# Kernel optimization log

Measured on AMD Instinct MI355X. Metric: run time of the kernel, lower is better.

The kernel has to match this reference:

```python
import jax, jax.numpy as jnp
import numpy as np

VAR0, VAR1 = 0.1, 0.2   # cfg['variance']
THRESH = 0.5            # overlap_thresh
THETA = 0.01
NEGPOS = 3


def decode(loc, priors):
    # priors center-form [P,4]; returns point-form boxes [P,4]
    cxcy = priors[:, :2] + loc[:, :2] * VAR0 * priors[:, 2:]
    wh = priors[:, 2:] * jnp.exp(loc[:, 2:] * VAR1)
    return jnp.concatenate([cxcy - wh * 0.5, cxcy + wh * 0.5], axis=1)


def center_size(b):
    return jnp.concatenate([(b[:, :2] + b[:, 2:]) * 0.5, b[:, 2:] - b[:, :2]], axis=1)


def encode(matched, priors_c):
    # matched point-form [P,4], priors_c center-form [P,4]
    g_cxcy = ((matched[:, :2] + matched[:, 2:]) * 0.5 - priors_c[:, :2]) / (VAR0 * priors_c[:, 2:])
    g_wh = jnp.log((matched[:, 2:] - matched[:, :2]) / priors_c[:, 2:]) / VAR1
    return jnp.concatenate([g_cxcy, g_wh], axis=1)


def jaccard(a, b):
    # a [G,4], b [P,4] point form -> IoU [G,P]
    lt = jnp.maximum(a[:, None, :2], b[None, :, :2])
    rb = jnp.minimum(a[:, None, 2:], b[None, :, 2:])
    wh = jnp.clip(rb - lt, 0.0)
    inter = wh[..., 0] * wh[..., 1]
    area_a = ((a[:, 2] - a[:, 0]) * (a[:, 3] - a[:, 1]))[:, None]
    area_b = ((b[:, 2] - b[:, 0]) * (b[:, 3] - b[:, 1]))[None, :]
    return inter / (area_a + area_b - inter)


def _match_one(truths, labels, gt_mask, arm_loc, priors):
    # refine_match with arm_loc (use_ARM=True path)
    P = priors.shape[0]
    G = truths.shape[0]
    dec = decode(arm_loc, priors)                                 # [P,4]
    ov = jnp.where(gt_mask[:, None], jaccard(truths, dec), -1.0)  # [G,P], padded GT masked out
    best_prior_idx = jnp.argmax(ov, axis=1)                       # [G]
    best_truth_ov = jnp.max(ov, axis=0)                           # [P]
    best_truth_idx = jnp.argmax(ov, axis=0)                       # [P]
    safe = jnp.where(gt_mask, best_prior_idx, P)                  # OOB index -> dropped scatter
    best_truth_ov = best_truth_ov.at[safe].set(2.0, mode='drop')  # force-match each valid GT
    best_truth_idx = best_truth_idx.at[safe].set(jnp.arange(G), mode='drop')
    matched = truths[best_truth_idx]                              # [P,4]
    conf = jnp.where(best_truth_ov < THRESH, 0, labels[best_truth_idx])
    loc = encode(matched, center_size(dec))
    return loc, conf


def forward(arm_loc, arm_conf, odm_loc, odm_conf, priors, targets, num_gts):
    B, P, C = odm_conf.shape
    truths = targets[..., :4]
    labels = targets[..., 4].astype(jnp.int32)
    gt_mask = jnp.arange(targets.shape[1])[None, :] < num_gts[:, None]
    loc_t, conf_t = jax.vmap(_match_one, in_axes=(0, 0, 0, 0, None))(
        truths, labels, gt_mask,
        jax.lax.stop_gradient(arm_loc), jax.lax.stop_gradient(priors))
    loc_t = jax.lax.stop_gradient(loc_t)    # loc_t.requires_grad = False
    conf_t = jax.lax.stop_gradient(conf_t)

    # ARM objectness filter on positives
    p_obj = jax.nn.softmax(arm_conf, axis=2)[:, :, 1]
    pos = (conf_t > 0) & (p_obj > THETA)

    # masked smooth-L1 localization loss (sum)
    posf = pos[..., None].astype(odm_loc.dtype)
    d = jnp.abs(odm_loc * posf - loc_t * posf)
    loss_l = jnp.sum(jnp.where(d < 1.0, 0.5 * d * d, d - 0.5))

    # hard negative mining on per-prior softmax loss
    batch_conf = odm_conf.reshape(-1, C)
    lc = jax.nn.logsumexp(batch_conf, axis=1) - jnp.take_along_axis(
        batch_conf, conf_t.reshape(-1, 1), axis=1)[:, 0]
    lc = jnp.where(pos.reshape(-1), 0.0, lc).reshape(B, P)
    loss_idx = jnp.argsort(-lc, axis=1)
    idx_rank = jnp.argsort(loss_idx, axis=1)
    num_pos = jnp.sum(pos.astype(jnp.int32), axis=1, keepdims=True)  # [B,1]
    num_neg = jnp.minimum(NEGPOS * num_pos, P - 1)
    neg = idx_rank < num_neg
    mask = pos | neg

    # masked cross entropy (compute on zeroed-out logits like the original, then mask)
    conf_p = (odm_conf * mask[..., None].astype(odm_conf.dtype)).reshape(-1, C)
    tgt = jnp.where(mask, conf_t, 0).reshape(-1)
    logp = jax.nn.log_softmax(conf_p, axis=1)
    ce = -jnp.take_along_axis(logp, tgt[:, None], axis=1)[:, 0]
    loss_c = jnp.sum(ce * mask.reshape(-1).astype(ce.dtype))

    N = jnp.sum(num_pos).astype(jnp.float32)
    return loss_l / N, loss_c / N


def setup_inputs():
    key = jax.random.key(0)
    ks = jax.random.split(key, 10)
    B, P, C, G = 32, 16320, 21, 40
    arm_loc = jax.random.normal(ks[0], (B, P, 4), jnp.float32) * 0.1
    arm_conf = jax.random.normal(ks[1], (B, P, 2), jnp.float32)
    odm_loc = jax.random.normal(ks[2], (B, P, 4), jnp.float32) * 0.1
    odm_conf = jax.random.normal(ks[3], (B, P, C), jnp.float32)
    # priors in center form with positive sizes
    pc = jax.random.uniform(ks[4], (P, 2), jnp.float32, 0.1, 0.9)
    pwh = jax.random.uniform(ks[5], (P, 2), jnp.float32, 0.05, 0.3)
    priors = jnp.concatenate([pc, pwh], axis=1)
    # GT boxes in point form with positive area, labels in 1..C-1, padded to G=40
    gc = jax.random.uniform(ks[6], (B, G, 2), jnp.float32, 0.2, 0.8)
    gwh = jax.random.uniform(ks[7], (B, G, 2), jnp.float32, 0.05, 0.3)
    boxes = jnp.concatenate([gc - gwh * 0.5, gc + gwh * 0.5], axis=-1)
    labels = jax.random.randint(ks[8], (B, G, 1), 1, C).astype(jnp.float32)
    targets = jnp.concatenate([boxes, labels], axis=-1)
    num_gts = jax.random.randint(ks[9], (B,), 1, G + 1).astype(jnp.int32)
    return {"arm_loc": arm_loc, "arm_conf": arm_conf, "odm_loc": odm_loc,
            "odm_conf": odm_conf, "priors": priors, "targets": targets,
            "num_gts": num_gts}


def reference(arm_loc, arm_conf, odm_loc, odm_conf, priors, targets, num_gts):
    return forward(arm_loc, arm_conf, odm_loc, odm_conf, priors, targets, num_gts)
```

## Files before the change

kernel.cpp:

```cpp
#include <hip/hip_runtime.h>
#include <math.h>

#define VAR0 0.1f
#define VAR1 0.2f
#define THRESH 0.5f
#define THETA 0.01f
#define MAXG 64
#define BLK 256
#define SELT 1024
#define NCH 16
#define NB 4096
#define CAP 2048

__device__ __forceinline__ float fdiv_fast(float a, float b) { return __fdividef(a, b); }

__device__ __forceinline__ float4 decode_box(float4 l, float4 pr) {
    float cx = pr.x + l.x * VAR0 * pr.z;
    float cy = pr.y + l.y * VAR0 * pr.w;
    float w = pr.z * __expf(l.z * VAR1);
    float h = pr.w * __expf(l.w * VAR1);
    return make_float4(cx - w * 0.5f, cy - h * 0.5f, cx + w * 0.5f, cy + h * 0.5f);
}

__device__ __forceinline__ float smooth_l1_sum(float4 ol, float4 t, float4 d) {
    float pcx = (d.x + d.z) * 0.5f, pcy = (d.y + d.w) * 0.5f;
    float pw = d.z - d.x, ph = d.w - d.y;
    float g0 = fdiv_fast((t.x + t.z) * 0.5f - pcx, VAR0 * pw);
    float g1 = fdiv_fast((t.y + t.w) * 0.5f - pcy, VAR0 * ph);
    float g2 = __logf(fdiv_fast(t.z - t.x, pw)) * (1.0f / VAR1);
    float g3 = __logf(fdiv_fast(t.w - t.y, ph)) * (1.0f / VAR1);
    float s = 0.f, dd;
    dd = fabsf(ol.x - g0); s += (dd < 1.f) ? 0.5f*dd*dd : dd - 0.5f;
    dd = fabsf(ol.y - g1); s += (dd < 1.f) ? 0.5f*dd*dd : dd - 0.5f;
    dd = fabsf(ol.z - g2); s += (dd < 1.f) ? 0.5f*dd*dd : dd - 0.5f;
    dd = fabsf(ol.w - g3); s += (dd < 1.f) ? 0.5f*dd*dd : dd - 0.5f;
    return s;
}

__device__ __forceinline__ float softmax_pobj(float2 c) {
    float mm = fmaxf(c.x, c.y);
    float e0 = __expf(c.x - mm), e1 = __expf(c.y - mm);
    return fdiv_fast(e1, e0 + e1);
}

__device__ __forceinline__ float iou_ov(float4 t, float areaA, float4 d, float areaB) {
    float lt0 = fmaxf(t.x, d.x), lt1 = fmaxf(t.y, d.y);
    float rb0 = fminf(t.z, d.z), rb1 = fminf(t.w, d.w);
    float w = rb0 - lt0; if (w < 0.f) w = 0.f;
    float h = rb1 - lt1; if (h < 0.f) h = 0.f;
    float inter = w * h;
    return fdiv_fast(inter, areaA + areaB - inter);
}

__device__ __forceinline__ unsigned wave_umax_bits(unsigned v) {
    int x = (int)v;
    int t;
    t = __builtin_amdgcn_update_dpp(0, x, 0x111, 0xf, 0xf, true);  x = (t > x) ? t : x;
    t = __builtin_amdgcn_update_dpp(0, x, 0x112, 0xf, 0xf, true);  x = (t > x) ? t : x;
    t = __builtin_amdgcn_update_dpp(0, x, 0x114, 0xf, 0xf, true);  x = (t > x) ? t : x;
    t = __builtin_amdgcn_update_dpp(0, x, 0x118, 0xf, 0xf, true);  x = (t > x) ? t : x;
    t = __builtin_amdgcn_update_dpp(0, x, 0x142, 0xa, 0xf, false); x = (t > x) ? t : x;
    t = __builtin_amdgcn_update_dpp(0, x, 0x143, 0xc, 0xf, false); x = (t > x) ? t : x;
    return (unsigned)__builtin_amdgcn_readlane(x, 63);
}

__global__ __launch_bounds__(BLK) void k_match(
        const float* __restrict__ arm_loc, const float* __restrict__ priors,
        const float* __restrict__ arm_conf, const float* __restrict__ odm_loc,
        const float* __restrict__ targets, const int* __restrict__ num_gts,
        unsigned char* __restrict__ posm, unsigned* __restrict__ bb,
        unsigned long long* __restrict__ bpw,
        float* __restrict__ partL, int* __restrict__ partN,
        int B, int P, int G) {
    int b = blockIdx.y;
    int p0 = blockIdx.x * BLK;
    int tid = threadIdx.x;
    int p = p0 + tid;
    int lane = tid & 63, wid = tid >> 6;
    int wavebase = p0 + (tid & ~63);
    __shared__ float4 st4[MAXG];
    __shared__ float  stl[MAXG];
    __shared__ float  sarea[MAXG];
    __shared__ unsigned long long wk[4][MAXG];
    __shared__ int sng;
    if (tid == 0) sng = num_gts[b];
    for (int g = tid; g < G; g += BLK) {
        const float* tg = targets + (size_t)b * G * 5 + g * 5;
        float t0 = tg[0], t1 = tg[1], t2 = tg[2], t3 = tg[3];
        st4[g] = make_float4(t0, t1, t2, t3);
        stl[g] = tg[4];
        sarea[g] = (t2 - t0) * (t3 - t1);
    }
    __syncthreads();
    int ng = sng;
    bool ok = p < P;
    float4 d = make_float4(0.f, 0.f, 0.f, 0.f);
    float areaB = 0.f;
    size_t i = (size_t)b * P + (ok ? p : 0);
    if (ok) {
        float4 l = ((const float4*)arm_loc)[i];
        float4 pr = ((const float4*)priors)[p];
        d = decode_box(l, pr);
        areaB = (d.z - d.x) * (d.w - d.y);
    }
    float bov = -2.0f; int bidx = 0;
    int g = 0;
    for (; g + 2 <= ng; g += 2) {
        float4 t0g = st4[g], t1g = st4[g + 1];
        unsigned vb0 = 0u, vb1 = 0u;
        if (ok) {
            float ov0 = iou_ov(t0g, sarea[g], d, areaB);
            float ov1 = iou_ov(t1g, sarea[g + 1], d, areaB);
            if (ov0 > bov) { bov = ov0; bidx = g; }
            if (ov1 > bov) { bov = ov1; bidx = g + 1; }
            vb0 = __float_as_uint(ov0);
            vb1 = __float_as_uint(ov1);
        }
        unsigned om0 = wave_umax_bits(vb0);
        unsigned om1 = wave_umax_bits(vb1);
        unsigned long long m0 = __ballot(ok && vb0 == om0);
        unsigned long long m1 = __ballot(ok && vb1 == om1);
        if (lane == 0) {
            unsigned long long k0 = 0ull, k1 = 0ull;
            if (m0) {
                int pw = wavebase + (int)__builtin_ctzll(m0);
                k0 = ((unsigned long long)om0 << 32)
                   | (unsigned long long)(0xFFFFFFFFu - (unsigned)pw);
            }
            if (m1) {
                int pw = wavebase + (int)__builtin_ctzll(m1);
                k1 = ((unsigned long long)om1 << 32)
                   | (unsigned long long)(0xFFFFFFFFu - (unsigned)pw);
            }
            wk[wid][g] = k0;
            wk[wid][g + 1] = k1;
        }
    }
    if (g < ng) {
        float4 tg = st4[g];
        unsigned vb = 0u;
        if (ok) {
            float ov = iou_ov(tg, sarea[g], d, areaB);
            if (ov > bov) { bov = ov; bidx = g; }
            vb = __float_as_uint(ov);
        }
        unsigned om = wave_umax_bits(vb);
        unsigned long long m = __ballot(ok && vb == om);
        if (lane == 0) {
            unsigned long long k0 = 0ull;
            if (m) {
                int pw = wavebase + (int)__builtin_ctzll(m);
                k0 = ((unsigned long long)om << 32)
                   | (unsigned long long)(0xFFFFFFFFu - (unsigned)pw);
            }
            wk[wid][g] = k0;
        }
    }
    float lsum = 0.f; int pc = 0;
    if (ok) {
        int conf_t = (bov < THRESH) ? 0 : (int)stl[bidx];
        float p_obj = softmax_pobj(((const float2*)arm_conf)[i]);
        bool pos = (conf_t > 0) && (p_obj > THETA);
        if (pos) {
            pc = 1;
            float4 ol = ((const float4*)odm_loc)[i];
            lsum = smooth_l1_sum(ol, st4[bidx], d);
        }
        posm[i] = pos ? 1 : 0;
        bb[i] = (__float_as_uint(bov) & 0xFFFFFFC0u) | (unsigned)bidx;
    }
    __shared__ float rl[BLK];
    __shared__ int rc[BLK];
    rl[tid] = lsum; rc[tid] = pc;
    __syncthreads();
    if (tid < ng) {
        unsigned long long k0 = wk[0][tid], k1 = wk[1][tid];
        unsigned long long k2 = wk[2][tid], k3 = wk[3][tid];
        unsigned long long m01 = k0 > k1 ? k0 : k1;
        unsigned long long m23 = k2 > k3 ? k2 : k3;
        unsigned long long m = m01 > m23 ? m01 : m23;
        bpw[(size_t)(b * G + tid) * gridDim.x + blockIdx.x] = m;
    }
    for (int off = BLK/2; off > 0; off >>= 1) {
        if (tid < off) { rl[tid] += rl[tid+off]; rc[tid] += rc[tid+off]; }
        __syncthreads();
    }
    if (tid == 0) {
        partL[b * gridDim.x + blockIdx.x] = rl[0];
        partN[b * gridDim.x + blockIdx.x] = rc[0];
    }
}

__global__ __launch_bounds__(BLK) void k_lse(
        const float* __restrict__ odm_conf, const float* __restrict__ targets,
        const unsigned* __restrict__ bb,
        float* __restrict__ ce, int B, int P, int C, int G) {
    int b = blockIdx.y;
    int p0 = blockIdx.x * BLK;
    int tid = threadIdx.x;
    int p = p0 + tid;
    __shared__ float stl[MAXG];
    __shared__ float oc_s[BLK * 21];
    for (int gg = tid; gg < G; gg += BLK) stl[gg] = targets[(size_t)b * G * 5 + gg * 5 + 4];
    int nrows = P - p0; if (nrows > BLK) nrows = BLK;
    int nf = nrows * C;
    const float* ocb = odm_conf + ((size_t)b * P + p0) * C;
    int nf4 = nf >> 2;
    const float4* ocb4 = (const float4*)ocb;
    for (int i2 = tid; i2 < nf4; i2 += BLK) ((float4*)oc_s)[i2] = ocb4[i2];
    if (tid < (nf & 3)) oc_s[(nf4 << 2) + tid] = ocb[(nf4 << 2) + tid];
    __syncthreads();
    if (p < P) {
        size_t i = (size_t)b * P + p;
        unsigned bbv = bb[i];
        int bidx = (int)(bbv & 63u);
        int conf_t = (__uint_as_float(bbv & 0xFFFFFFC0u) >= THRESH) ? (int)stl[bidx] : 0;
        const float* oc = oc_s + tid * C;
        float mx = oc[0];
        for (int j = 1; j < C; ++j) mx = fmaxf(mx, oc[j]);
        float sume = 0.f;
        for (int j = 0; j < C; ++j) sume += __expf(oc[j] - mx);
        float lse = mx + __logf(sume);
        ce[i] = lse - oc[conf_t];
    }
}

__global__ __launch_bounds__(1024) void k_fixpatch(
        const float* __restrict__ arm_loc, const float* __restrict__ priors,
        const float* __restrict__ arm_conf, const float* __restrict__ odm_loc,
        const float* __restrict__ odm_conf,
        const float* __restrict__ targets, const int* __restrict__ num_gts,
        const unsigned long long* __restrict__ bpw, const unsigned* __restrict__ bb,
        float* __restrict__ ce, unsigned char* __restrict__ posm,
        float* __restrict__ partPL, int* __restrict__ partPN,
        int B, int P, int C, int G, int NBX) {
    int b = blockIdx.x;
    int tid = threadIdx.x;
    int lane = tid & 63, wid = tid >> 6;
    __shared__ int fp[MAXG];
    __shared__ float4 st4[MAXG];
    __shared__ float  stl[MAXG];
    __shared__ int sng;
    if (tid == 0) sng = num_gts[b];
    for (int g = tid; g < G; g += 1024) {
        const float* tg = targets + (size_t)b * G * 5 + g * 5;
        st4[g] = make_float4(tg[0], tg[1], tg[2], tg[3]);
        stl[g] = tg[4];
    }
    __syncthreads();
    int ng = sng;
    for (int g = wid; g < ng; g += 16) {
        const unsigned long long* src = bpw + (size_t)(b * G + g) * NBX;
        unsigned long long key = 0ull;
        for (int j = lane; j < NBX; j += 64) {
            unsigned long long v = src[j];
            if (v > key) key = v;
        }
        for (int off = 32; off > 0; off >>= 1) {
            unsigned long long o = __shfl_down(key, (unsigned)off, 64);
            if (o > key) key = o;
        }
        if (lane == 0) fp[g] = (int)(0xFFFFFFFFu - (unsigned)(key & 0xFFFFFFFFull));
    }
    __syncthreads();
    if (tid < G) {
        float dL = 0.f; int dN = 0;
        if (tid < ng) {
            int g = tid;
            bool dup = false;
            for (int g2 = g + 1; g2 < ng; ++g2) if (fp[g2] == fp[g]) { dup = true; break; }
            if (!dup) {
                int p = fp[g];
                size_t i = (size_t)b * P + p;
                unsigned bbv = bb[i];
                int old_bidx = (int)(bbv & 63u);
                bool old_ge = __uint_as_float(bbv & 0xFFFFFFC0u) >= THRESH;
                int old_ct = old_ge ? (int)stl[old_bidx] : 0;
                int new_ct = (int)stl[g];
                float p_obj = softmax_pobj(((const float2*)arm_conf)[i]);
                bool old_pos = (old_ct > 0) && (p_obj > THETA);
                bool new_pos = (p_obj > THETA);
                if (old_pos || new_pos) {
                    float4 l = ((const float4*)arm_loc)[i];
                    float4 pr = ((const float4*)priors)[p];
                    float4 d = decode_box(l, pr);
                    float4 ol = ((const float4*)odm_loc)[i];
                    if (old_pos) dL -= smooth_l1_sum(ol, st4[old_bidx], d);
                    if (new_pos) dL += smooth_l1_sum(ol, st4[g], d);
                }
                dN = (new_pos ? 1 : 0) - (old_pos ? 1 : 0);
                const float* oc = odm_conf + i * (size_t)C;
                float ce_old = ce[i];
                float ce_new = (old_ct == new_ct) ? ce_old
                             : (ce_old + oc[old_ct] - oc[new_ct]);
                ce[i] = ce_new;
                posm[i] = new_pos ? 1 : 0;
            }
        }
        partPL[b * G + tid] = dL;
        partPN[b * G + tid] = dN;
    }
}

__global__ __launch_bounds__(SELT) void k_select(
        const float* __restrict__ ce, const unsigned char* __restrict__ posm,
        const int* __restrict__ partN, const int* __restrict__ partPN,
        const float* __restrict__ partL, const float* __restrict__ partPL,
        int NBX, int G,
        float* __restrict__ partC, float* __restrict__ totL,
        int* __restrict__ npos, int P) {
    int b = blockIdx.x;
    int tid = threadIdx.x;
    int lane = tid & 63, wid = tid >> 6;
    __shared__ unsigned hist[NB];
    __shared__ float cv[CAP];
    __shared__ int   ci[CAP];
    __shared__ int   sums[SELT];
    __shared__ int   redi[16];
    __shared__ float redf[16];
    __shared__ int sh_base[16];
    __shared__ int sh_m, sh_b1, sh_k1, sh_npos, sh_istar, sh_kk, sh_cum;
    __shared__ unsigned sh_T, sh_pref;
    __shared__ float sh_mx, sh_totl;

    int c0 = 0; float l0 = 0.f;
    for (int j = tid; j < NBX; j += SELT) { c0 += partN[b * NBX + j]; l0 += partL[b * NBX + j]; }
    for (int g = tid; g < G; g += SELT)   { c0 += partPN[b * G + g];  l0 += partPL[b * G + g]; }
    for (int off = 32; off > 0; off >>= 1) {
        c0 += __shfl_down(c0, (unsigned)off, 64);
        l0 += __shfl_down(l0, (unsigned)off, 64);
    }
    if (lane == 0) { redi[wid] = c0; redf[wid] = l0; }
    __syncthreads();
    if (tid < 64) {
        int v = (tid < 16) ? redi[tid] : 0;
        float f = (tid < 16) ? redf[tid] : 0.f;
        for (int off = 32; off > 0; off >>= 1) {
            v += __shfl_down(v, (unsigned)off, 64);
            f += __shfl_down(f, (unsigned)off, 64);
        }
        if (tid == 0) { sh_npos = v; sh_totl = f; }
    }
    __syncthreads();
    int npos_b = sh_npos;
    long K = 3L * npos_b;
    if (K > P - 1) K = P - 1;

    unsigned cb[NCH];
    unsigned lv[NCH];
    unsigned pmw = 0u;
    const unsigned* ceb = (const unsigned*)ce + (size_t)b * P;
    const unsigned char* pb = posm + (size_t)b * P;
    #pragma unroll
    for (int c = 0; c < NCH; ++c) {
        int i = c * SELT + tid;
        unsigned cbits = (i < P) ? ceb[i] : 0u;
        bool ps = (i < P) && (pb[i] != 0);
        cb[c] = cbits;
        if (ps) pmw |= (1u << c);
        lv[c] = ps ? 0u : cbits;
    }

    unsigned uT = 0xFFFFFFFFu; int istar = -1;
    if (K > 0) {
        float mx = 0.f;
        #pragma unroll
        for (int c = 0; c < NCH; ++c) mx = fmaxf(mx, __uint_as_float(lv[c]));
        for (int off = 32; off > 0; off >>= 1) mx = fmaxf(mx, __shfl_xor(mx, off, 64));
        if (lane == 0) redf[wid] = mx;
        __syncthreads();
        if (tid == 0) {
            float v = redf[0];
            for (int w = 1; w < 16; ++w) v = fmaxf(v, redf[w]);
            sh_mx = v;
        }
        __syncthreads();
        float vmax = sh_mx;
        float scale = (vmax > 0.f) ? ((float)NB / vmax) : 0.f;

        for (int j = tid; j < NB; j += SELT) hist[j] = 0u;
        __syncthreads();
        #pragma unroll
        for (int c = 0; c < NCH; ++c) {
            int i = c * SELT + tid;
            if (i < P) {
                int bn = (int)(__uint_as_float(lv[c]) * scale);
                if (bn > NB - 1) bn = NB - 1;
                atomicAdd(&hist[bn], 1u);
            }
        }
        __syncthreads();

        int s4 = (int)(hist[4*tid] + hist[4*tid+1] + hist[4*tid+2] + hist[4*tid+3]);
        sums[SELT - 1 - tid] = s4;
        __syncthreads();
        int x = sums[tid];
        int xs = x;
        for (int off = 1; off < 64; off <<= 1) {
            int o = __shfl_up(xs, (unsigned)off, 64);
            if (lane >= off) xs += o;
        }
        if (lane == 63) redi[wid] = xs;
        __syncthreads();
        if (tid < 64) {
            int v = (tid < 16) ? redi[tid] : 0;
            int vs = v;
            for (int off = 1; off < 16; off <<= 1) {
                int o = __shfl_up(vs, (unsigned)off, 64);
                if (lane >= off) vs += o;
            }
            if (tid < 16) redi[tid] = vs - v;
        }
        __syncthreads();
        int excl_rev = xs + redi[wid] - x;
        sums[tid] = excl_rev;
        __syncthreads();
        int suf = sums[SELT - 1 - tid];
        {
            int run = suf;
            for (int j = 3; j >= 0; --j) {
                int bin = 4 * tid + j;
                int h = (int)hist[bin];
                if ((long)run < K && K <= (long)run + h) { sh_b1 = bin; sh_k1 = (int)(K - run); }
                run += h;
            }
        }
        __syncthreads();
        int B1 = sh_b1, k1 = sh_k1;

        if (tid == 0) sh_m = 0;
        __syncthreads();
        #pragma unroll
        for (int c = 0; c < NCH; ++c) {
            int i = c * SELT + tid;
            if (i < P) {
                float f = __uint_as_float(lv[c]);
                int bn = (int)(f * scale);
                if (bn > NB - 1) bn = NB - 1;
                if (bn == B1) {
                    int pos = atomicAdd(&sh_m, 1);
                    if (pos < CAP) { cv[pos] = f; ci[pos] = i; }
                }
            }
        }
        __syncthreads();
        int m = sh_m;
        if (m <= CAP) {
            for (int j = tid; j < m; j += SELT) {
                float vj = cv[j]; int ij = ci[j]; int r = 0;
                for (int jj = 0; jj < m; ++jj) {
                    float vx = cv[jj];
                    r += (vx > vj || (vx == vj && ci[jj] < ij)) ? 1 : 0;
                }
                if (r == k1 - 1) { sh_T = __float_as_uint(vj); sh_istar = ij; }
            }
            __syncthreads();
            uT = sh_T; istar = sh_istar;
        } else {
            if (tid == 0) { sh_pref = 0u; sh_kk = (int)K; }
            __syncthreads();
            for (int bit = 30; bit >= 0; --bit) {
                unsigned pref = sh_pref;
                int kk = sh_kk;
                unsigned hi = pref >> (bit + 1);
                int cnt = 0;
                #pragma unroll
                for (int c = 0; c < NCH; ++c) {
                    int i = c * SELT + tid;
                    unsigned v = lv[c];
                    cnt += ((i < P) && ((v >> (bit + 1)) == hi) && ((v >> bit) & 1u)) ? 1 : 0;
                }
                for (int off = 32; off > 0; off >>= 1) cnt += __shfl_down(cnt, (unsigned)off, 64);
                if (lane == 0) redi[wid] = cnt;
                __syncthreads();
                if (tid < 64) {
                    int v = (tid < 16) ? redi[tid] : 0;
                    for (int off = 32; off > 0; off >>= 1) v += __shfl_down(v, (unsigned)off, 64);
                    if (tid == 0) {
                        if (kk <= v) sh_pref = pref | (1u << bit);
                        else sh_kk = kk - v;
                    }
                }
                __syncthreads();
            }
            unsigned T = sh_pref; int krem = sh_kk;
            if (tid == 0) { sh_istar = -1; sh_cum = 0; }
            __syncthreads();
            for (int c = 0; c < NCH; ++c) {
                int i = c * SELT + tid;
                bool eq = (i < P) && (lv[c] == T);
                unsigned long long mk = __ballot(eq);
                if (lane == 0) redi[wid] = (int)__popcll(mk);
                __syncthreads();
                if (tid < 64) {
                    int v = (tid < 16) ? redi[tid] : 0;
                    for (int off = 1; off < 16; off <<= 1) {
                        int o = __shfl_up(v, (unsigned)off, 64);
                        if (lane >= off) v += o;
                    }
                    if (tid < 16) sh_base[tid] = v;
                }
                __syncthreads();
                int cum = sh_cum;
                int base = (wid == 0) ? 0 : sh_base[wid - 1];
                if (eq) {
                    int r = cum + base + (int)__popcll(mk & ((1ull << lane) - 1ull));
                    if (r == krem - 1) sh_istar = i;
                }
                __syncthreads();
                if (tid == 0) sh_cum = cum + sh_base[15];
                __syncthreads();
                if (sh_cum >= krem) break;
            }
            __syncthreads();
            uT = T; istar = sh_istar;
        }
    }

    float cs = 0.f;
    #pragma unroll
    for (int c = 0; c < NCH; ++c) {
        int i = c * SELT + tid;
        if (i < P) {
            unsigned v = lv[c];
            bool sel = ((pmw >> c) & 1u) || (v > uT) || (v == uT && i <= istar);
            if (sel) cs += __uint_as_float(cb[c]);
        }
    }
    for (int off = 32; off > 0; off >>= 1) cs += __shfl_down(cs, (unsigned)off, 64);
    if (lane == 0) redf[wid] = cs;
    __syncthreads();
    if (tid < 64) {
        float v = (tid < 16) ? redf[tid] : 0.f;
        for (int off = 32; off > 0; off >>= 1) v += __shfl_down(v, (unsigned)off, 64);
        if (tid == 0) { partC[b] = v; npos[b] = npos_b; totL[b] = sh_totl; }
    }
}

__global__ void k_final(const float* __restrict__ totL, const float* __restrict__ partC,
                        const int* __restrict__ npos, float* __restrict__ out, int B) {
    int tid = threadIdx.x;
    float aL = (tid < B) ? totL[tid] : 0.f;
    float aC = (tid < B) ? partC[tid] : 0.f;
    int   aN = (tid < B) ? npos[tid] : 0;
    for (int off = 32; off > 0; off >>= 1) {
        aL += __shfl_down(aL, (unsigned)off, 64);
        aC += __shfl_down(aC, (unsigned)off, 64);
        aN += __shfl_down(aN, (unsigned)off, 64);
    }
    if (tid == 0) {
        float N = (float)aN;
        out[0] = aL / N;
        out[1] = aC / N;
    }
}

extern "C" void kernel_launch(void* const* d_in, const int* in_sizes, int n_in,
                              void* d_out, int out_size, void* d_ws, size_t ws_size,
                              hipStream_t stream) {
    const float* arm_loc  = (const float*)d_in[0];
    const float* arm_conf = (const float*)d_in[1];
    const float* odm_loc  = (const float*)d_in[2];
    const float* odm_conf = (const float*)d_in[3];
    const float* priors   = (const float*)d_in[4];
    const float* targets  = (const float*)d_in[5];
    const int*   num_gts  = (const int*)d_in[6];
    float* out = (float*)d_out;

    int B = in_sizes[6];
    int P = in_sizes[4] / 4;
    int C = in_sizes[3] / (B * P);
    int G = in_sizes[5] / (B * 5);
    int NBX = (P + BLK - 1) / BLK;

    char* ws = (char*)d_ws;
    size_t off = 0;
    auto alloc = [&](size_t bytes) -> void* {
        void* ptr = ws + off;
        off = (off + bytes + 255) & ~(size_t)255;
        return ptr;
    };
    unsigned long long* bpw = (unsigned long long*)alloc((size_t)B * G * NBX * 8);
    unsigned* bb = (unsigned*)alloc((size_t)B * P * 4);
    float* ce  = (float*)alloc((size_t)B * P * sizeof(float));
    unsigned char* posm = (unsigned char*)alloc((size_t)B * P);
    float* partL = (float*)alloc((size_t)B * NBX * sizeof(float));
    int* partN   = (int*)alloc((size_t)B * NBX * sizeof(int));
    float* partPL = (float*)alloc((size_t)B * G * sizeof(float));
    int* partPN   = (int*)alloc((size_t)B * G * sizeof(int));
    float* partC = (float*)alloc((size_t)B * sizeof(float));
    float* totL  = (float*)alloc((size_t)B * sizeof(float));
    int* npos    = (int*)alloc((size_t)B * sizeof(int));

    k_match<<<dim3(NBX, B), BLK, 0, stream>>>(arm_loc, priors, arm_conf, odm_loc, targets,
                                              num_gts, posm, bb, bpw, partL, partN, B, P, G);
    k_lse<<<dim3(NBX, B), BLK, 0, stream>>>(odm_conf, targets, bb, ce, B, P, C, G);
    k_fixpatch<<<B, 1024, 0, stream>>>(arm_loc, priors, arm_conf, odm_loc, odm_conf,
                                       targets, num_gts, bpw, bb, ce, posm,
                                       partPL, partPN, B, P, C, G, NBX);
    k_select<<<B, SELT, 0, stream>>>(ce, posm, partN, partPN, partL, partPL,
                                     NBX, G, partC, totL, npos, P);
    k_final<<<1, 64, 0, stream>>>(totL, partC, npos, out, B);
}
```

Baseline: 64.53 us.

## Fuse match with log-sum-exp, merge fixpatch/select/final into one tail kernel

Merges the matching kernel and the cross-entropy log-sum-exp kernel so odm_conf rows are prefetched into registers during IoU matching and staged to LDS afterwards. The per-GT fixpatch, hard-negative selection and final reduction are combined into a single per-batch kernel, and the last block finishes the global reduction using an atomic counter. This cuts five launches to two and removes the bb round trip, at the cost of more LDS and registers per block (possible occupancy loss) and a counter reset that depends on launch ordering.

```diff
diff --git a/kernel.cpp b/kernel.cpp
--- a/kernel.cpp
+++ b/kernel.cpp
@@ -11,6 +11,7 @@
 #define NCH 16
 #define NB 4096
 #define CAP 2048
+#define NST 6
 
 __device__ __forceinline__ float fdiv_fast(float a, float b) { return __fdividef(a, b); }
 
@@ -64,14 +65,15 @@
     return (unsigned)__builtin_amdgcn_readlane(x, 63);
 }
 
-__global__ __launch_bounds__(BLK) void k_match(
+__global__ __launch_bounds__(BLK) void k_main2(
         const float* __restrict__ arm_loc, const float* __restrict__ priors,
         const float* __restrict__ arm_conf, const float* __restrict__ odm_loc,
+        const float* __restrict__ odm_conf,
         const float* __restrict__ targets, const int* __restrict__ num_gts,
-        unsigned char* __restrict__ posm, unsigned* __restrict__ bb,
-        unsigned long long* __restrict__ bpw,
-        float* __restrict__ partL, int* __restrict__ partN,
-        int B, int P, int G) {
+        float* __restrict__ ce, unsigned char* __restrict__ posm,
+        unsigned* __restrict__ bb, unsigned long long* __restrict__ bpw,
+        float* __restrict__ partL, int* __restrict__ partN, int* __restrict__ counter,
+        int B, int P, int C, int G) {
     int b = blockIdx.y;
     int p0 = blockIdx.x * BLK;
     int tid = threadIdx.x;
@@ -82,7 +84,11 @@
     __shared__ float  stl[MAXG];
     __shared__ float  sarea[MAXG];
     __shared__ unsigned long long wk[4][MAXG];
+    __shared__ float oc_s[BLK * 21];
+    __shared__ float rl[BLK];
+    __shared__ int   rc[BLK];
     __shared__ int sng;
+    if (blockIdx.x == 0 && blockIdx.y == 0 && tid == 0) *counter = 0;
     if (tid == 0) sng = num_gts[b];
     for (int g = tid; g < G; g += BLK) {
         const float* tg = targets + (size_t)b * G * 5 + g * 5;
@@ -92,6 +98,18 @@
         sarea[g] = (t2 - t0) * (t3 - t1);
     }
     __syncthreads();
+
+    int nrows = P - p0; if (nrows > BLK) nrows = BLK;
+    int nf = nrows * C;
+    int nf4 = nf >> 2;
+    const float4* ocb4 = (const float4*)(odm_conf + ((size_t)b * P + p0) * C);
+    float4 stg[NST];
+    #pragma unroll
+    for (int r = 0; r < NST; ++r) {
+        int idx = r * BLK + tid;
+        stg[r] = (idx < nf4) ? ocb4[idx] : make_float4(0.f, 0.f, 0.f, 0.f);
+    }
+
     int ng = sng;
     bool ok = p < P;
     float4 d = make_float4(0.f, 0.f, 0.f, 0.f);
@@ -156,9 +174,11 @@
             wk[wid][g] = k0;
         }
     }
+
     float lsum = 0.f; int pc = 0;
+    int conf_t = 0;
     if (ok) {
-        int conf_t = (bov < THRESH) ? 0 : (int)stl[bidx];
+        conf_t = (bov < THRESH) ? 0 : (int)stl[bidx];
         float p_obj = softmax_pobj(((const float2*)arm_conf)[i]);
         bool pos = (conf_t > 0) && (p_obj > THETA);
         if (pos) {
@@ -169,10 +189,16 @@
         posm[i] = pos ? 1 : 0;
         bb[i] = (__float_as_uint(bov) & 0xFFFFFFC0u) | (unsigned)bidx;
     }
-    __shared__ float rl[BLK];
-    __shared__ int rc[BLK];
     rl[tid] = lsum; rc[tid] = pc;
-    __syncthreads();
+
+    #pragma unroll
+    for (int r = 0; r < NST; ++r) {
+        int idx = r * BLK + tid;
+        if (idx < nf4) ((float4*)oc_s)[idx] = stg[r];
+    }
+    for (int t = (nf4 << 2) + tid; t < nf; t += BLK) oc_s[t] = ((const float*)ocb4)[t];
+    __syncthreads();
+
     if (tid < ng) {
         unsigned long long k0 = wk[0][tid], k1 = wk[1][tid];
         unsigned long long k2 = wk[2][tid], k3 = wk[3][tid];
@@ -181,40 +207,8 @@
         unsigned long long m = m01 > m23 ? m01 : m23;
         bpw[(size_t)(b * G + tid) * gridDim.x + blockIdx.x] = m;
     }
-    for (int off = BLK/2; off > 0; off >>= 1) {
-        if (tid < off) { rl[tid] += rl[tid+off]; rc[tid] += rc[tid+off]; }
-        __syncthreads();
-    }
-    if (tid == 0) {
-        partL[b * gridDim.x + blockIdx.x] = rl[0];
-        partN[b * gridDim.x + blockIdx.x] = rc[0];
-    }
-}
-
-__global__ __launch_bounds__(BLK) void k_lse(
-        const float* __restrict__ odm_conf, const float* __restrict__ targets,
-        const unsigned* __restrict__ bb,
-        float* __restrict__ ce, int B, int P, int C, int G) {
-    int b = blockIdx.y;
-    int p0 = blockIdx.x * BLK;
-    int tid = threadIdx.x;
-    int p = p0 + tid;
-    __shared__ float stl[MAXG];
-    __shared__ float oc_s[BLK * 21];
-    for (int gg = tid; gg < G; gg += BLK) stl[gg] = targets[(size_t)b * G * 5 + gg * 5 + 4];
-    int nrows = P - p0; if (nrows > BLK) nrows = BLK;
-    int nf = nrows * C;
-    const float* ocb = odm_conf + ((size_t)b * P + p0) * C;
-    int nf4 = nf >> 2;
-    const float4* ocb4 = (const float4*)ocb;
-    for (int i2 = tid; i2 < nf4; i2 += BLK) ((float4*)oc_s)[i2] = ocb4[i2];
-    if (tid < (nf & 3)) oc_s[(nf4 << 2) + tid] = ocb[(nf4 << 2) + tid];
-    __syncthreads();
-    if (p < P) {
-        size_t i = (size_t)b * P + p;
-        unsigned bbv = bb[i];
-        int bidx = (int)(bbv & 63u);
-        int conf_t = (__uint_as_float(bbv & 0xFFFFFFC0u) >= THRESH) ? (int)stl[bidx] : 0;
+
+    if (ok) {
         const float* oc = oc_s + tid * C;
         float mx = oc[0];
         for (int j = 1; j < C; ++j) mx = fmaxf(mx, oc[j]);
@@ -223,95 +217,36 @@
         float lse = mx + __logf(sume);
         ce[i] = lse - oc[conf_t];
     }
-}
-
-__global__ __launch_bounds__(1024) void k_fixpatch(
+
+    for (int off = BLK / 2; off > 0; off >>= 1) {
+        if (tid < off) { rl[tid] += rl[tid + off]; rc[tid] += rc[tid + off]; }
+        __syncthreads();
+    }
+    if (tid == 0) {
+        partL[b * gridDim.x + blockIdx.x] = rl[0];
+        partN[b * gridDim.x + blockIdx.x] = rc[0];
+    }
+}
+
+__global__ __launch_bounds__(SELT) void k_tail(
         const float* __restrict__ arm_loc, const float* __restrict__ priors,
         const float* __restrict__ arm_conf, const float* __restrict__ odm_loc,
         const float* __restrict__ odm_conf,
         const float* __restrict__ targets, const int* __restrict__ num_gts,
         const unsigned long long* __restrict__ bpw, const unsigned* __restrict__ bb,
         float* __restrict__ ce, unsigned char* __restrict__ posm,
-        float* __restrict__ partPL, int* __restrict__ partPN,
-        int B, int P, int C, int G, int NBX) {
+        const float* __restrict__ partL, const int* __restrict__ partN,
+        float* __restrict__ partC, float* __restrict__ totL, int* __restrict__ npos,
+        int* __restrict__ counter, float* __restrict__ out,
+        int NBX, int B, int P, int C, int G) {
     int b = blockIdx.x;
     int tid = threadIdx.x;
     int lane = tid & 63, wid = tid >> 6;
     __shared__ int fp[MAXG];
     __shared__ float4 st4[MAXG];
     __shared__ float  stl[MAXG];
-    __shared__ int sng;
-    if (tid == 0) sng = num_gts[b];
-    for (int g = tid; g < G; g += 1024) {
-        const float* tg = targets + (size_t)b * G * 5 + g * 5;
-        st4[g] = make_float4(tg[0], tg[1], tg[2], tg[3]);
-        stl[g] = tg[4];
-    }
-    __syncthreads();
-    int ng = sng;
-    for (int g = wid; g < ng; g += 16) {
-        const unsigned long long* src = bpw + (size_t)(b * G + g) * NBX;
-        unsigned long long key = 0ull;
-        for (int j = lane; j < NBX; j += 64) {
-            unsigned long long v = src[j];
-            if (v > key) key = v;
-        }
-        for (int off = 32; off > 0; off >>= 1) {
-            unsigned long long o = __shfl_down(key, (unsigned)off, 64);
-            if (o > key) key = o;
-        }
-        if (lane == 0) fp[g] = (int)(0xFFFFFFFFu - (unsigned)(key & 0xFFFFFFFFull));
-    }
-    __syncthreads();
-    if (tid < G) {
-        float dL = 0.f; int dN = 0;
-        if (tid < ng) {
-            int g = tid;
-            bool dup = false;
-            for (int g2 = g + 1; g2 < ng; ++g2) if (fp[g2] == fp[g]) { dup = true; break; }
-            if (!dup) {
-                int p = fp[g];
-                size_t i = (size_t)b * P + p;
-                unsigned bbv = bb[i];
-                int old_bidx = (int)(bbv & 63u);
-                bool old_ge = __uint_as_float(bbv & 0xFFFFFFC0u) >= THRESH;
-                int old_ct = old_ge ? (int)stl[old_bidx] : 0;
-                int new_ct = (int)stl[g];
-                float p_obj = softmax_pobj(((const float2*)arm_conf)[i]);
-                bool old_pos = (old_ct > 0) && (p_obj > THETA);
-                bool new_pos = (p_obj > THETA);
-                if (old_pos || new_pos) {
-                    float4 l = ((const float4*)arm_loc)[i];
-                    float4 pr = ((const float4*)priors)[p];
-                    float4 d = decode_box(l, pr);
-                    float4 ol = ((const float4*)odm_loc)[i];
-                    if (old_pos) dL -= smooth_l1_sum(ol, st4[old_bidx], d);
-                    if (new_pos) dL += smooth_l1_sum(ol, st4[g], d);
-                }
-                dN = (new_pos ? 1 : 0) - (old_pos ? 1 : 0);
-                const float* oc = odm_conf + i * (size_t)C;
-                float ce_old = ce[i];
-                float ce_new = (old_ct == new_ct) ? ce_old
-                             : (ce_old + oc[old_ct] - oc[new_ct]);
-                ce[i] = ce_new;
-                posm[i] = new_pos ? 1 : 0;
-            }
-        }
-        partPL[b * G + tid] = dL;
-        partPN[b * G + tid] = dN;
-    }
-}
-
-__global__ __launch_bounds__(SELT) void k_select(
-        const float* __restrict__ ce, const unsigned char* __restrict__ posm,
-        const int* __restrict__ partN, const int* __restrict__ partPN,
-        const float* __restrict__ partL, const float* __restrict__ partPL,
-        int NBX, int G,
-        float* __restrict__ partC, float* __restrict__ totL,
-        int* __restrict__ npos, int P) {
-    int b = blockIdx.x;
-    int tid = threadIdx.x;
-    int lane = tid & 63, wid = tid >> 6;
+    __shared__ float  pdl[MAXG];
+    __shared__ int    pdn[MAXG];
     __shared__ unsigned hist[NB];
     __shared__ float cv[CAP];
     __shared__ int   ci[CAP];
@@ -319,13 +254,74 @@
     __shared__ int   redi[16];
     __shared__ float redf[16];
     __shared__ int sh_base[16];
-    __shared__ int sh_m, sh_b1, sh_k1, sh_npos, sh_istar, sh_kk, sh_cum;
+    __shared__ int sh_m, sh_b1, sh_k1, sh_npos, sh_istar, sh_kk, sh_cum, sh_last;
     __shared__ unsigned sh_T, sh_pref;
     __shared__ float sh_mx, sh_totl;
+    __shared__ int sng;
+    if (tid == 0) sng = num_gts[b];
+    for (int g = tid; g < G; g += SELT) {
+        const float* tg = targets + (size_t)b * G * 5 + g * 5;
+        st4[g] = make_float4(tg[0], tg[1], tg[2], tg[3]);
+        stl[g] = tg[4];
+        pdl[g] = 0.f; pdn[g] = 0;
+    }
+    __syncthreads();
+    int ng = sng;
+
+    for (int g = wid; g < ng; g += 16) {
+        const unsigned long long* src = bpw + (size_t)(b * G + g) * NBX;
+        unsigned long long key = 0ull;
+        for (int j = lane; j < NBX; j += 64) {
+            unsigned long long v = src[j];
+            if (v > key) key = v;
+        }
+        for (int off = 32; off > 0; off >>= 1) {
+            unsigned long long o = __shfl_down(key, (unsigned)off, 64);
+            if (o > key) key = o;
+        }
+        if (lane == 0) fp[g] = (int)(0xFFFFFFFFu - (unsigned)(key & 0xFFFFFFFFull));
+    }
+    __syncthreads();
+
+    if (tid < ng) {
+        int g = tid;
+        bool dup = false;
+        for (int g2 = g + 1; g2 < ng; ++g2) if (fp[g2] == fp[g]) { dup = true; break; }
+        if (!dup) {
+            int p = fp[g];
+            size_t i = (size_t)b * P + p;
+            unsigned bbv = bb[i];
+            int old_bidx = (int)(bbv & 63u);
+            bool old_ge = __uint_as_float(bbv & 0xFFFFFFC0u) >= THRESH;
+            int old_ct = old_ge ? (int)stl[old_bidx] : 0;
+            int new_ct = (int)stl[g];
+            float p_obj = softmax_pobj(((const float2*)arm_conf)[i]);
+            bool old_pos = (old_ct > 0) && (p_obj > THETA);
+            bool new_pos = (p_obj > THETA);
+            float dL = 0.f;
+            if (old_pos || new_pos) {
+                float4 l = ((const float4*)arm_loc)[i];
+                float4 pr = ((const float4*)priors)[p];
+                float4 d = decode_box(l, pr);
+                float4 ol = ((const float4*)odm_loc)[i];
+                if (old_pos) dL -= smooth_l1_sum(ol, st4[old_bidx], d);
+                if (new_pos) dL += smooth_l1_sum(ol, st4[g], d);
+            }
+            pdl[g] = dL;
+            pdn[g] = (new_pos ? 1 : 0) - (old_pos ? 1 : 0);
+            const float* oc = odm_conf + i * (size_t)C;
+            float ce_old = ce[i];
+            float ce_new = (old_ct == new_ct) ? ce_old
+                         : (ce_old + oc[old_ct] - oc[new_ct]);
+            ce[i] = ce_new;
+            posm[i] = new_pos ? 1 : 0;
+        }
+    }
+    __syncthreads();
 
     int c0 = 0; float l0 = 0.f;
     for (int j = tid; j < NBX; j += SELT) { c0 += partN[b * NBX + j]; l0 += partL[b * NBX + j]; }
-    for (int g = tid; g < G; g += SELT)   { c0 += partPN[b * G + g];  l0 += partPL[b * G + g]; }
+    for (int g = tid; g < G; g += SELT)   { c0 += pdn[g];             l0 += pdl[g]; }
     for (int off = 32; off > 0; off >>= 1) {
         c0 += __shfl_down(c0, (unsigned)off, 64);
         l0 += __shfl_down(l0, (unsigned)off, 64);
@@ -533,25 +529,32 @@
     if (tid < 64) {
         float v = (tid < 16) ? redf[tid] : 0.f;
         for (int off = 32; off > 0; off >>= 1) v += __shfl_down(v, (unsigned)off, 64);
-        if (tid == 0) { partC[b] = v; npos[b] = npos_b; totL[b] = sh_totl; }
-    }
-}
-
-__global__ void k_final(const float* __restrict__ totL, const float* __restrict__ partC,
-                        const int* __restrict__ npos, float* __restrict__ out, int B) {
-    int tid = threadIdx.x;
-    float aL = (tid < B) ? totL[tid] : 0.f;
-    float aC = (tid < B) ? partC[tid] : 0.f;
-    int   aN = (tid < B) ? npos[tid] : 0;
-    for (int off = 32; off > 0; off >>= 1) {
-        aL += __shfl_down(aL, (unsigned)off, 64);
-        aC += __shfl_down(aC, (unsigned)off, 64);
-        aN += __shfl_down(aN, (unsigned)off, 64);
-    }
-    if (tid == 0) {
-        float N = (float)aN;
-        out[0] = aL / N;
-        out[1] = aC / N;
+        if (tid == 0) {
+            partC[b] = v; npos[b] = npos_b; totL[b] = sh_totl;
+            __threadfence();
+            int old = atomicAdd(counter, 1);
+            sh_last = (old == B - 1) ? 1 : 0;
+        }
+    }
+    __syncthreads();
+
+    if (sh_last && tid < 64) {
+        float aL = 0.f, aC = 0.f; int aN = 0;
+        if (tid < B) {
+            aL = atomicAdd(&totL[tid], 0.0f);
+            aC = atomicAdd(&partC[tid], 0.0f);
+            aN = atomicAdd(&npos[tid], 0);
+        }
+        for (int off = 32; off > 0; off >>= 1) {
+            aL += __shfl_down(aL, (unsigned)off, 64);
+            aC += __shfl_down(aC, (unsigned)off, 64);
+            aN += __shfl_down(aN, (unsigned)off, 64);
+        }
+        if (tid == 0) {
+            float N = (float)aN;
+            out[0] = aL / N;
+            out[1] = aC / N;
+        }
     }
 }
 
@@ -586,19 +589,16 @@
     unsigned char* posm = (unsigned char*)alloc((size_t)B * P);
     float* partL = (float*)alloc((size_t)B * NBX * sizeof(float));
     int* partN   = (int*)alloc((size_t)B * NBX * sizeof(int));
-    float* partPL = (float*)alloc((size_t)B * G * sizeof(float));
-    int* partPN   = (int*)alloc((size_t)B * G * sizeof(int));
     float* partC = (float*)alloc((size_t)B * sizeof(float));
     float* totL  = (float*)alloc((size_t)B * sizeof(float));
     int* npos    = (int*)alloc((size_t)B * sizeof(int));
-
-    k_match<<<dim3(NBX, B), BLK, 0, stream>>>(arm_loc, priors, arm_conf, odm_loc, targets,
-                                              num_gts, posm, bb, bpw, partL, partN, B, P, G);
-    k_lse<<<dim3(NBX, B), BLK, 0, stream>>>(odm_conf, targets, bb, ce, B, P, C, G);
-    k_fixpatch<<<B, 1024, 0, stream>>>(arm_loc, priors, arm_conf, odm_loc, odm_conf,
-                                       targets, num_gts, bpw, bb, ce, posm,
-                                       partPL, partPN, B, P, C, G, NBX);
-    k_select<<<B, SELT, 0, stream>>>(ce, posm, partN, partPN, partL, partPL,
-                                     NBX, G, partC, totL, npos, P);
-    k_final<<<1, 64, 0, stream>>>(totL, partC, npos, out, B);
-}
+    int* counter = (int*)alloc(sizeof(int));
+
+    k_main2<<<dim3(NBX, B), BLK, 0, stream>>>(arm_loc, priors, arm_conf, odm_loc, odm_conf,
+                                              targets, num_gts, ce, posm, bb, bpw,
+                                              partL, partN, counter, B, P, C, G);
+    k_tail<<<B, SELT, 0, stream>>>(arm_loc, priors, arm_conf, odm_loc, odm_conf,
+                                   targets, num_gts, bpw, bb, ce, posm,
+                                   partL, partN, partC, totL, npos, counter, out,
+                                   NBX, B, P, C, G);
+}
```

Result: faster. 58.40 us (-9.5%).
